# Performance work log

Measured on AMD Instinct MI355X. Metric: run time of the kernel, lower is better.

## Reference

```python
import jax, jax.numpy as jnp
import numpy as np

DIM = 512
WIN = 7
HEADS = 16
N = WIN * WIN            # 49 tokens per window
NW = 64                  # windows per image (56/7)^2
BATCH = 32               # images
B_ = BATCH * NW          # 2048 window-batches
TABLE = (2 * WIN - 1) ** 2  # 169


def _relative_position_index(win):
    # Faithful to the TF construction in __init__.
    coords = np.stack(np.meshgrid(np.arange(win), np.arange(win), indexing='ij'))
    coords = coords.reshape(2, -1).T                      # [N, 2]
    rel = coords[:, None, :] - coords[None, :, :]          # [N, N, 2]
    rel = rel + (win - 1)
    idx = rel[..., 0] * (2 * win - 1) + rel[..., 1]        # [N, N]
    return jnp.asarray(idx, dtype=jnp.int32)


def setup_inputs() -> dict:
    key = jax.random.key(0)
    ks = jax.random.split(key, 7)
    x = jax.random.normal(ks[0], (B_, N, DIM), dtype=jnp.float32)
    # shifted-window additive mask: 0 where allowed, -100 where blocked
    mask = jnp.where(jax.random.uniform(ks[1], (NW, N, N)) < 0.8, 0.0, -100.0).astype(jnp.float32)
    qkv_w = jax.random.normal(ks[2], (DIM, 3 * DIM), dtype=jnp.float32) * 0.02
    qkv_b = jax.random.normal(ks[3], (3 * DIM,), dtype=jnp.float32) * 0.02
    proj_w = jax.random.normal(ks[4], (DIM, DIM), dtype=jnp.float32) * 0.02
    proj_b = jax.random.normal(ks[5], (DIM,), dtype=jnp.float32) * 0.02
    rel_table = jax.random.normal(ks[6], (TABLE, HEADS), dtype=jnp.float32) * 0.02
    rel_index = _relative_position_index(WIN)
    return {"x": x, "mask": mask, "qkv_w": qkv_w, "qkv_b": qkv_b,
            "proj_w": proj_w, "proj_b": proj_b,
            "rel_table": rel_table, "rel_index": rel_index}


def reference(x, mask, qkv_w, qkv_b, proj_w, proj_b, rel_table, rel_index):
    B, n, C = x.shape
    hd = C // HEADS
    scale = hd ** (-0.5)
    # qkv projection -> [3, B, H, N, hd]
    qkv = (x @ qkv_w + qkv_b).reshape(B, n, 3, HEADS, hd).transpose(2, 0, 3, 1, 4)
    q, k, v = qkv[0] * scale, qkv[1], qkv[2]
    attn = jnp.einsum('bhnd,bhmd->bhnm', q, k)             # [B, H, N, N]
    # relative position bias gather: [N*N] -> [N, N, H] -> [H, N, N]
    bias = rel_table[rel_index.reshape(-1)].reshape(n, n, HEADS).transpose(2, 0, 1)
    attn = attn + bias[None]
    nW = mask.shape[0]
    attn = attn.reshape(B // nW, nW, HEADS, n, n) + mask[None, :, None]
    attn = attn.reshape(-1, HEADS, n, n)
    attn = jax.nn.softmax(attn, axis=-1)
    out = jnp.einsum('bhnm,bhmd->bhnd', attn, v)           # [B, H, N, hd]
    out = out.transpose(0, 2, 1, 3).reshape(B, n, C)
    return out @ proj_w + proj_b
```

## Files before the change

### kernel.cpp

```cpp
#include <hip/hip_runtime.h>

typedef unsigned short ushort_t;
typedef short short8 __attribute__((ext_vector_type(8)));
typedef float f32x4 __attribute__((ext_vector_type(4)));
typedef unsigned short ushort4v __attribute__((ext_vector_type(4)));

__device__ __forceinline__ ushort_t f2bf(float f) {
    unsigned int u = __float_as_uint(f);
    u = (u + 0x7fffu + ((u >> 16) & 1u)) >> 16;
    return (ushort_t)u;
}

__device__ __forceinline__ void async16(void* lds, const void* g) {
    __builtin_amdgcn_global_load_lds(
        (const __attribute__((address_space(1))) unsigned int*)g,
        (__attribute__((address_space(3))) unsigned int*)lds, 16, 0, 0);
}

__global__ void conv_x_kernel(const float* __restrict__ in, ushort_t* __restrict__ out) {
    int i = blockIdx.x * 256 + threadIdx.x;
    float4 v = ((const float4*)in)[i];
    ushort4v o;
    o.x = f2bf(v.x); o.y = f2bf(v.y); o.z = f2bf(v.z); o.w = f2bf(v.w);
    ((ushort4v*)out)[i] = o;
}

__global__ void prep_weights(const float* __restrict__ qkv_w, const float* __restrict__ proj_w,
                             ushort_t* __restrict__ wtq, ushort_t* __restrict__ wtp) {
    int o = blockIdx.x * 256 + threadIdx.x;
    if (o < 1536 * 512) {
        int n = o >> 9, k = o & 511;
        wtq[o] = f2bf(qkv_w[k * 1536 + n]);
    }
    if (o < 512 * 512) {
        int n = o >> 9, k = o & 511;
        wtp[o] = f2bf(proj_w[k * 512 + n]);
    }
}

__global__ void build_cm(const float* __restrict__ mask, const float* __restrict__ rel_table,
                         const int* __restrict__ rel_index, float* __restrict__ cm) {
    int o = blockIdx.x * 256 + threadIdx.x;
    int c = o & 63, r = (o >> 6) & 63, h = (o >> 12) & 15, w = o >> 16;
    float v = -30000.0f;
    if (r < 49 && c < 49)
        v = rel_table[rel_index[r * 49 + c] * 16 + h] + mask[w * 2401 + r * 49 + c];
    cm[o] = v;
}

template<int NSTR, bool QKV>
__global__ __launch_bounds__(256, 2)
void gemm_bt(const ushort_t* __restrict__ A, const ushort_t* __restrict__ Bt,
             const float* __restrict__ bias, void* __restrict__ out,
             int M, int K)
{
    __shared__ alignas(16) ushort_t As[128 * 32];
    __shared__ alignas(16) ushort_t Bs[128 * 32];
    const int tid = threadIdx.x;
    const int wid = tid >> 6;
    const int lane = tid & 63;
    const int lr = lane & 15;
    const int lk = lane >> 4;
    const int m0 = blockIdx.x << 7;
    const int n0 = blockIdx.y << 7;
    const int wr = (wid >> 1) << 6;
    const int wc = (wid & 1) << 6;

    f32x4 acc[4][4];
#pragma unroll
    for (int i = 0; i < 4; ++i)
#pragma unroll
        for (int j = 0; j < 4; ++j)
#pragma unroll
            for (int r = 0; r < 4; ++r) acc[i][j][r] = 0.f;

    const int KT = K >> 5;
    for (int kt = 0; kt < KT; ++kt) {
        const int kb = kt << 5;
#pragma unroll
        for (int t = 0; t < 2; ++t) {
            const int cb = t * 256 + wid * 64;
            const int c = cb + lane;
            async16((char*)As + cb * 16, A + (size_t)(m0 + (c >> 2)) * K + kb + (c & 3) * 8);
            async16((char*)Bs + cb * 16, Bt + (size_t)(n0 + (c >> 2)) * K + kb + (c & 3) * 8);
        }
        __syncthreads();
        short8 af[4], bf[4];
#pragma unroll
        for (int i = 0; i < 4; ++i) af[i] = *(const short8*)&As[(wr + i * 16 + lr) * 32 + lk * 8];
#pragma unroll
        for (int j = 0; j < 4; ++j) bf[j] = *(const short8*)&Bs[(wc + j * 16 + lr) * 32 + lk * 8];
#pragma unroll
        for (int i = 0; i < 4; ++i)
#pragma unroll
            for (int j = 0; j < 4; ++j)
                acc[i][j] = __builtin_amdgcn_mfma_f32_16x16x32_bf16(af[i], bf[j], acc[i][j], 0, 0, 0);
        __syncthreads();
    }

#pragma unroll
    for (int j = 0; j < 4; ++j) {
        const int col = n0 + wc + j * 16 + lr;
        const float bv = bias[col];
#pragma unroll
        for (int i = 0; i < 4; ++i) {
#pragma unroll
            for (int r = 0; r < 4; ++r) {
                const int row = m0 + wr + i * 16 + lk * 4 + r;
                float v = acc[i][j][r] + bv;
                if (QKV) {
                    if (col < 512) v *= 0.17677669529663689f;
                    ((ushort_t*)out)[(size_t)row * NSTR + col] = f2bf(v);
                } else {
                    ((float*)out)[(size_t)row * NSTR + col] = v;
                }
            }
        }
    }
}

#define PL_STRIDE 80
#define VT_STRIDE 88
__global__ __launch_bounds__(256, 2)
void attn_kernel(const ushort_t* __restrict__ qkv, const float* __restrict__ cm,
                 ushort_t* __restrict__ out)
{
    __shared__ alignas(16) char smem[4 * 64 * PL_STRIDE * 2 + 4 * 32 * VT_STRIDE * 2];
    float* cmf = (float*)smem;
    ushort_t* Pl = (ushort_t*)smem;
    ushort_t* vT = (ushort_t*)(smem + 4 * 64 * PL_STRIDE * 2);

    const int w = blockIdx.x, h = blockIdx.y, ig = blockIdx.z;
    const int tid = threadIdx.x;
    const int wid = tid >> 6, lane = tid & 63;
    const int lr = lane & 15, lk = lane >> 4;
    const int b = (ig * 4 + wid) * 64 + w;

    const float* cmsrc = cm + ((size_t)(w * 16 + h) << 12);
    for (int t = tid; t < 4096; t += 256)
        cmf[(t >> 6) * 65 + (t & 63)] = cmsrc[t];
    __syncthreads();

    const size_t base = (size_t)b * 49 * 1536 + h * 32;

    short8 aq[4], bk[4];
#pragma unroll
    for (int i = 0; i < 4; ++i) {
        int n = i * 16 + lr; n = n > 48 ? 48 : n;
        aq[i] = *(const short8*)&qkv[base + (size_t)n * 1536 + lk * 8];
    }
#pragma unroll
    for (int j = 0; j < 4; ++j) {
        int m = j * 16 + lr; m = m > 48 ? 48 : m;
        bk[j] = *(const short8*)&qkv[base + 512 + (size_t)m * 1536 + lk * 8];
    }

    f32x4 s[4][4];
#pragma unroll
    for (int i = 0; i < 4; ++i)
#pragma unroll
        for (int j = 0; j < 4; ++j)
#pragma unroll
            for (int r = 0; r < 4; ++r) s[i][j][r] = 0.f;
#pragma unroll
    for (int i = 0; i < 4; ++i)
#pragma unroll
        for (int j = 0; j < 4; ++j)
            s[i][j] = __builtin_amdgcn_mfma_f32_16x16x32_bf16(aq[i], bk[j], s[i][j], 0, 0, 0);

    short8 vv[4];
#pragma unroll
    for (int t = 0; t < 4; ++t)
#pragma unroll
        for (int e = 0; e < 8; ++e) vv[t][e] = 0;
    if (lane < 49) {
        const ushort_t* vp = &qkv[base + 1024 + (size_t)lane * 1536];
#pragma unroll
        for (int t = 0; t < 4; ++t) vv[t] = *(const short8*)(vp + t * 8);
    }
    ushort_t* vTw = vT + wid * 32 * VT_STRIDE;
#pragma unroll
    for (int t = 0; t < 4; ++t)
#pragma unroll
        for (int e = 0; e < 8; ++e)
            vTw[(t * 8 + e) * VT_STRIDE + lane] = (ushort_t)vv[t][e];

#pragma unroll
    for (int i = 0; i < 4; ++i) {
#pragma unroll
        for (int r = 0; r < 4; ++r) {
            const int row = i * 16 + lk * 4 + r;
            float v0 = s[i][0][r] + cmf[row * 65 + lr];
            float v1 = s[i][1][r] + cmf[row * 65 + 16 + lr];
            float v2 = s[i][2][r] + cmf[row * 65 + 32 + lr];
            float v3 = s[i][3][r] + cmf[row * 65 + 48 + lr];
            float mx = fmaxf(fmaxf(v0, v1), fmaxf(v2, v3));
#pragma unroll
            for (int t = 1; t < 16; t <<= 1) mx = fmaxf(mx, __shfl_xor(mx, t, 64));
            v0 = __expf(v0 - mx); v1 = __expf(v1 - mx);
            v2 = __expf(v2 - mx); v3 = __expf(v3 - mx);
            float sm = v0 + v1 + v2 + v3;
#pragma unroll
            for (int t = 1; t < 16; t <<= 1) sm += __shfl_xor(sm, t, 64);
            const float inv = 1.0f / sm;
            s[i][0][r] = v0 * inv; s[i][1][r] = v1 * inv;
            s[i][2][r] = v2 * inv; s[i][3][r] = v3 * inv;
        }
    }
    __syncthreads();

    ushort_t* Pw = Pl + wid * 64 * PL_STRIDE;
#pragma unroll
    for (int i = 0; i < 4; ++i)
#pragma unroll
        for (int j = 0; j < 4; ++j)
#pragma unroll
            for (int r = 0; r < 4; ++r)
                Pw[(i * 16 + lk * 4 + r) * PL_STRIDE + j * 16 + lr] = f2bf(s[i][j][r]);

    f32x4 o[4][2];
#pragma unroll
    for (int i = 0; i < 4; ++i)
#pragma unroll
        for (int jb = 0; jb < 2; ++jb)
#pragma unroll
            for (int r = 0; r < 4; ++r) o[i][jb][r] = 0.f;
#pragma unroll
    for (int ks = 0; ks < 2; ++ks) {
        short8 pa[4], vb[2];
#pragma unroll
        for (int i = 0; i < 4; ++i)
            pa[i] = *(const short8*)&Pw[(i * 16 + lr) * PL_STRIDE + ks * 32 + lk * 8];
#pragma unroll
        for (int jb = 0; jb < 2; ++jb)
            vb[jb] = *(const short8*)&vTw[(jb * 16 + lr) * VT_STRIDE + ks * 32 + lk * 8];
#pragma unroll
        for (int i = 0; i < 4; ++i)
#pragma unroll
            for (int jb = 0; jb < 2; ++jb)
                o[i][jb] = __builtin_amdgcn_mfma_f32_16x16x32_bf16(pa[i], vb[jb], o[i][jb], 0, 0, 0);
    }

    const size_t obase = (size_t)b * 49 * 512 + h * 32;
#pragma unroll
    for (int i = 0; i < 4; ++i) {
#pragma unroll
        for (int r = 0; r < 4; ++r) {
            const int n = i * 16 + lk * 4 + r;
            if (n < 49) {
#pragma unroll
                for (int jb = 0; jb < 2; ++jb)
                    out[obase + (size_t)n * 512 + jb * 16 + lr] = f2bf(o[i][jb][r]);
            }
        }
    }
}

extern "C" void kernel_launch(void* const* d_in, const int* in_sizes, int n_in,
                              void* d_out, int out_size, void* d_ws, size_t ws_size,
                              hipStream_t stream)
{
    const float* x         = (const float*)d_in[0];
    const float* mask      = (const float*)d_in[1];
    const float* qkv_w     = (const float*)d_in[2];
    const float* qkv_b     = (const float*)d_in[3];
    const float* proj_w    = (const float*)d_in[4];
    const float* proj_b    = (const float*)d_in[5];
    const float* rel_table = (const float*)d_in[6];
    const int*   rel_index = (const int*)d_in[7];

    char* ws = (char*)d_ws;
    ushort_t* xb  = (ushort_t*)ws;
    ushort_t* qkv = (ushort_t*)(ws + 102760448);
    ushort_t* wtq = (ushort_t*)(ws + 411041792);
    ushort_t* wtp = (ushort_t*)(ws + 412614656);
    float*    cm  = (float*)  (ws + 413138944);

    conv_x_kernel<<<50176, 256, 0, stream>>>(x, xb);
    prep_weights<<<3072, 256, 0, stream>>>(qkv_w, proj_w, wtq, wtp);
    build_cm<<<16384, 256, 0, stream>>>(mask, rel_table, rel_index, cm);

    gemm_bt<1536, true><<<dim3(784, 12), 256, 0, stream>>>(xb, wtq, qkv_b, qkv, 100352, 512);

    attn_kernel<<<dim3(64, 16, 8), 256, 0, stream>>>(qkv, cm, xb);

    gemm_bt<512, false><<<dim3(784, 4), 256, 0, stream>>>(xb, wtp, proj_b, d_out, 100352, 512);
}
```

Measured before the change: 629.6 us.

## Swizzle GEMM LDS tiles, transpose MFMA outputs for vector stores, reorder grids

```diff
diff --git a/kernel.cpp b/kernel.cpp
--- a/kernel.cpp
+++ b/kernel.cpp
@@ -61,8 +61,8 @@
     const int lane = tid & 63;
     const int lr = lane & 15;
     const int lk = lane >> 4;
-    const int m0 = blockIdx.x << 7;
-    const int n0 = blockIdx.y << 7;
+    const int n0 = blockIdx.x << 7;
+    const int m0 = blockIdx.y << 7;
     const int wr = (wid >> 1) << 6;
     const int wc = (wid & 1) << 6;
 
@@ -81,39 +81,48 @@
         for (int t = 0; t < 2; ++t) {
             const int cb = t * 256 + wid * 64;
             const int c = cb + lane;
-            async16((char*)As + cb * 16, A + (size_t)(m0 + (c >> 2)) * K + kb + (c & 3) * 8);
-            async16((char*)Bs + cb * 16, Bt + (size_t)(n0 + (c >> 2)) * K + kb + (c & 3) * 8);
+            const int row = c >> 2;
+            const int kc = (c & 3) ^ ((row >> 1) & 3);
+            async16((char*)As + cb * 16, A + (size_t)(m0 + row) * K + kb + kc * 8);
+            async16((char*)Bs + cb * 16, Bt + (size_t)(n0 + row) * K + kb + kc * 8);
         }
         __syncthreads();
+        const int swz = ((lr >> 1) & 3) << 3;
         short8 af[4], bf[4];
 #pragma unroll
-        for (int i = 0; i < 4; ++i) af[i] = *(const short8*)&As[(wr + i * 16 + lr) * 32 + lk * 8];
-#pragma unroll
-        for (int j = 0; j < 4; ++j) bf[j] = *(const short8*)&Bs[(wc + j * 16 + lr) * 32 + lk * 8];
+        for (int i = 0; i < 4; ++i) af[i] = *(const short8*)&As[(wr + i * 16 + lr) * 32 + ((lk * 8) ^ swz)];
+#pragma unroll
+        for (int j = 0; j < 4; ++j) bf[j] = *(const short8*)&Bs[(wc + j * 16 + lr) * 32 + ((lk * 8) ^ swz)];
 #pragma unroll
         for (int i = 0; i < 4; ++i)
 #pragma unroll
             for (int j = 0; j < 4; ++j)
-                acc[i][j] = __builtin_amdgcn_mfma_f32_16x16x32_bf16(af[i], bf[j], acc[i][j], 0, 0, 0);
+                acc[i][j] = __builtin_amdgcn_mfma_f32_16x16x32_bf16(bf[j], af[i], acc[i][j], 0, 0, 0);
         __syncthreads();
     }
 
 #pragma unroll
-    for (int j = 0; j < 4; ++j) {
-        const int col = n0 + wc + j * 16 + lr;
-        const float bv = bias[col];
-#pragma unroll
-        for (int i = 0; i < 4; ++i) {
-#pragma unroll
-            for (int r = 0; r < 4; ++r) {
-                const int row = m0 + wr + i * 16 + lk * 4 + r;
-                float v = acc[i][j][r] + bv;
-                if (QKV) {
-                    if (col < 512) v *= 0.17677669529663689f;
-                    ((ushort_t*)out)[(size_t)row * NSTR + col] = f2bf(v);
-                } else {
-                    ((float*)out)[(size_t)row * NSTR + col] = v;
+    for (int i = 0; i < 4; ++i) {
+        const int row = m0 + wr + i * 16 + lr;
+#pragma unroll
+        for (int j = 0; j < 4; ++j) {
+            const int col = n0 + wc + j * 16 + lk * 4;
+            const float4 bv = *(const float4*)&bias[col];
+            float v0 = acc[i][j][0] + bv.x;
+            float v1 = acc[i][j][1] + bv.y;
+            float v2 = acc[i][j][2] + bv.z;
+            float v3 = acc[i][j][3] + bv.w;
+            if (QKV) {
+                if (col < 512) {
+                    v0 *= 0.17677669529663689f; v1 *= 0.17677669529663689f;
+                    v2 *= 0.17677669529663689f; v3 *= 0.17677669529663689f;
                 }
+                ushort4v o;
+                o.x = f2bf(v0); o.y = f2bf(v1); o.z = f2bf(v2); o.w = f2bf(v3);
+                *(ushort4v*)&((ushort_t*)out)[(size_t)row * NSTR + col] = o;
+            } else {
+                float4 o; o.x = v0; o.y = v1; o.z = v2; o.w = v3;
+                *(float4*)&((float*)out)[(size_t)row * NSTR + col] = o;
             }
         }
     }
@@ -130,7 +139,7 @@
     ushort_t* Pl = (ushort_t*)smem;
     ushort_t* vT = (ushort_t*)(smem + 4 * 64 * PL_STRIDE * 2);
 
-    const int w = blockIdx.x, h = blockIdx.y, ig = blockIdx.z;
+    const int ig = blockIdx.x, w = blockIdx.y, h = blockIdx.z;
     const int tid = threadIdx.x;
     const int wid = tid >> 6, lane = tid & 63;
     const int lr = lane & 15, lk = lane >> 4;
@@ -238,19 +247,20 @@
         for (int i = 0; i < 4; ++i)
 #pragma unroll
             for (int jb = 0; jb < 2; ++jb)
-                o[i][jb] = __builtin_amdgcn_mfma_f32_16x16x32_bf16(pa[i], vb[jb], o[i][jb], 0, 0, 0);
+                o[i][jb] = __builtin_amdgcn_mfma_f32_16x16x32_bf16(vb[jb], pa[i], o[i][jb], 0, 0, 0);
     }
 
     const size_t obase = (size_t)b * 49 * 512 + h * 32;
 #pragma unroll
     for (int i = 0; i < 4; ++i) {
-#pragma unroll
-        for (int r = 0; r < 4; ++r) {
-            const int n = i * 16 + lk * 4 + r;
-            if (n < 49) {
-#pragma unroll
-                for (int jb = 0; jb < 2; ++jb)
-                    out[obase + (size_t)n * 512 + jb * 16 + lr] = f2bf(o[i][jb][r]);
+        const int n = i * 16 + lr;
+        if (n < 49) {
+#pragma unroll
+            for (int jb = 0; jb < 2; ++jb) {
+                ushort4v ov;
+                ov.x = f2bf(o[i][jb][0]); ov.y = f2bf(o[i][jb][1]);
+                ov.z = f2bf(o[i][jb][2]); ov.w = f2bf(o[i][jb][3]);
+                *(ushort4v*)&out[obase + (size_t)n * 512 + jb * 16 + lk * 4] = ov;
             }
         }
     }
@@ -280,9 +290,9 @@
     prep_weights<<<3072, 256, 0, stream>>>(qkv_w, proj_w, wtq, wtp);
     build_cm<<<16384, 256, 0, stream>>>(mask, rel_table, rel_index, cm);
 
-    gemm_bt<1536, true><<<dim3(784, 12), 256, 0, stream>>>(xb, wtq, qkv_b, qkv, 100352, 512);
-
-    attn_kernel<<<dim3(64, 16, 8), 256, 0, stream>>>(qkv, cm, xb);
-
-    gemm_bt<512, false><<<dim3(784, 4), 256, 0, stream>>>(xb, wtp, proj_b, d_out, 100352, 512);
-}
+    gemm_bt<1536, true><<<dim3(12, 784), 256, 0, stream>>>(xb, wtq, qkv_b, qkv, 100352, 512);
+
+    attn_kernel<<<dim3(8, 64, 16), 256, 0, stream>>>(qkv, cm, xb);
+
+    gemm_bt<512, false><<<dim3(4, 784), 256, 0, stream>>>(xb, wtp, proj_b, d_out, 100352, 512);
+}
```

After: 671.9 us. 1.07x slower.
